# Performance work log

Measured on AMD Instinct MI355X. Metric: run time of the kernel, lower is better.

## Reference

```python
import jax, jax.numpy as jnp
import numpy as np

N = 100000          # num nodes
E = 1250000         # num directed edges
F_IN = 64           # num_features
H = 64              # hidden_channels
C = 2               # num_classes


def gcn_layer(x, W, b, src, dst, num_nodes):
    """PyG-style GCNConv: add self-loops, symmetric norm, scatter-add aggregation."""
    loop = jnp.arange(num_nodes)
    src2 = jnp.concatenate([src, loop])   # [E+N]
    dst2 = jnp.concatenate([dst, loop])
    deg = jax.ops.segment_sum(jnp.ones_like(dst2, dtype=x.dtype), dst2,
                              num_segments=num_nodes)          # in-degree incl self-loop
    dinv = jax.lax.rsqrt(jnp.maximum(deg, 1.0))                # deg >= 1 due to self-loops
    norm = dinv[src2] * dinv[dst2]                             # [E+N]
    h = x @ W                                                  # [N, out]
    out = jax.ops.segment_sum(norm[:, None] * h[src2], dst2,
                              num_segments=num_nodes)          # [N, out]
    return out + b


def setup_inputs() -> dict:
    key = jax.random.key(0)
    ks = jax.random.split(key, 8)
    x = jax.random.normal(ks[0], (N, F_IN), dtype=jnp.float32)
    edge_index = jax.random.randint(ks[1], (2, E), 0, N, dtype=jnp.int64)
    batch = jnp.zeros((N,), dtype=jnp.int64)
    s1 = 1.0 / np.sqrt(F_IN)
    s2 = 1.0 / np.sqrt(H)
    W1 = jax.random.uniform(ks[2], (F_IN, H), jnp.float32, -s1, s1)
    b1 = jnp.zeros((H,), jnp.float32)
    W2 = jax.random.uniform(ks[3], (H, H), jnp.float32, -s2, s2)
    b2 = jnp.zeros((H,), jnp.float32)
    Wlin = jax.random.uniform(ks[4], (H, C), jnp.float32, -s2, s2)
    blin = jax.random.uniform(ks[5], (C,), jnp.float32, -s2, s2)
    return {"x": x, "edge_index": edge_index, "batch": batch,
            "W1": W1, "b1": b1, "W2": W2, "b2": b2,
            "Wlin": Wlin, "blin": blin}


def reference(x, edge_index, batch, W1, b1, W2, b2, Wlin, blin):
    src, dst = edge_index[0], edge_index[1]
    h = gcn_layer(x, W1, b1, src, dst, N)
    h = jax.nn.relu(h)
    h = gcn_layer(h, W2, b2, src, dst, N)
    # dropout p=0.5 is identity in eval mode
    return h @ Wlin + blin  # [N, C]
```

## Files before the change

kernel.cpp:

```cpp
#include <hip/hip_runtime.h>
#include <hip/hip_bf16.h>


#define FDIM 64
#define BKT_BITS 9
#define BKT 512
#define CAP 8192
#define CHUNK 2048

typedef short s16x8 __attribute__((ext_vector_type(8)));
typedef float f32x4 __attribute__((ext_vector_type(4)));

__device__ __forceinline__ unsigned short f2b(float f) {
    unsigned u = __float_as_uint(f);
    u += 0x7fff + ((u >> 16) & 1);
    return (unsigned short)(u >> 16);
}
__device__ __forceinline__ void unpk(unsigned u, float& lo, float& hi) {
    lo = __uint_as_float(u << 16);
    hi = __uint_as_float(u & 0xffff0000u);
}
__device__ __forceinline__ unsigned packb(float lo, float hi) {
    return (unsigned)f2b(lo) | ((unsigned)f2b(hi) << 16);
}
__device__ __forceinline__ unsigned relu2(unsigned u) {
    unsigned t = (u >> 15) & 0x00010001u;
    return u & ~(t * 0xFFFFu);
}

__global__ __launch_bounds__(256) void k_zero_g(int* __restrict__ g, int nb) {
    int i = blockIdx.x * blockDim.x + threadIdx.x;
    if (i < nb) g[i] = 0;
}

__global__ __launch_bounds__(256) void k_part(const int* __restrict__ src,
                                              const int* __restrict__ dst,
                                              int* __restrict__ gcnt,
                                              unsigned* __restrict__ rec,
                                              int nE, int nb) {
    __shared__ int lh[256];
    __shared__ int rc[256];
    int t = threadIdx.x;
    if (t < nb) lh[t] = 0;
    __syncthreads();
    int e0 = blockIdx.x * CHUNK;
    int e1 = min(nE, e0 + CHUNK);
    int myb[8];
    unsigned myr[8];
#pragma unroll
    for (int j = 0; j < 8; ++j) {
        int i = e0 + t + j * 256;
        if (i < e1) {
            int d = dst[i];
            int s = src[i];
            int b = d >> BKT_BITS;
            myb[j] = b;
            myr[j] = (unsigned)s | ((unsigned)(d & (BKT - 1)) << 17);
            atomicAdd(&lh[b], 1);
        } else {
            myb[j] = -1;
        }
    }
    __syncthreads();
    if (t < nb) {
        int c = lh[t];
        rc[t] = t * CAP + (c ? atomicAdd(&gcnt[t], c) : 0);
    }
    __syncthreads();
#pragma unroll
    for (int j = 0; j < 8; ++j) {
        int b = myb[j];
        if (b >= 0) {
            int pos = atomicAdd(&rc[b], 1);
            if (pos < (b + 1) * CAP)
                rec[pos] = myr[j];
        }
    }
}

__global__ __launch_bounds__(256) void k_bscan(const int* __restrict__ gcnt,
                                               int* __restrict__ base,
                                               int* __restrict__ rowptr,
                                               int nb, int nE, int n) {
    int t = threadIdx.x;
    int b0 = t * 4;
    int v[4];
    int run = 0;
#pragma unroll
    for (int j = 0; j < 4; ++j) {
        int idx = b0 + j;
        int c = (idx < nb) ? gcnt[idx] : 0;
        v[j] = run;
        run += c;
    }
    int lane = t & 63, w = t >> 6;
    int inc = run;
#pragma unroll
    for (int off = 1; off < 64; off <<= 1) {
        int x = __shfl_up(inc, off);
        if (lane >= off) inc += x;
    }
    __shared__ int wt[4];
    if (lane == 63) wt[w] = inc;
    __syncthreads();
    int woff = 0;
    for (int i = 0; i < w; ++i) woff += wt[i];
    int gb = woff + (inc - run);
#pragma unroll
    for (int j = 0; j < 4; ++j) {
        int idx = b0 + j;
        if (idx < nb) base[idx] = gb + v[j];
    }
    if (t == 0) { base[nb] = nE; rowptr[n] = nE; }
}

__global__ __launch_bounds__(256) void k_bfill(const unsigned* __restrict__ rec,
                                               const int* __restrict__ gcnt,
                                               const int* __restrict__ base,
                                               int* __restrict__ rowptr,
                                               float* __restrict__ dinv,
                                               int* __restrict__ col, int n) {
    __shared__ int deg[BKT];
    __shared__ int cur[BKT];
    __shared__ int wt[4];
    int b = blockIdx.x, t = threadIdx.x;
    deg[t] = 0;
    deg[t + 256] = 0;
    __syncthreads();
    int rb = b * CAP;
    int re = rb + min(gcnt[b], CAP);
    for (int i = rb + t; i < re; i += 256)
        atomicAdd(&deg[rec[i] >> 17], 1);
    __syncthreads();
    {
        int d0 = deg[2 * t], d1 = deg[2 * t + 1];
        int run = d0 + d1;
        int lane = t & 63, w = t >> 6;
        int inc = run;
#pragma unroll
        for (int off = 1; off < 64; off <<= 1) {
            int x = __shfl_up(inc, off);
            if (lane >= off) inc += x;
        }
        if (lane == 63) wt[w] = inc;
        __syncthreads();
        int woff = 0;
        for (int i = 0; i < w; ++i) woff += wt[i];
        int ex = base[b] + woff + (inc - run);
        int off0 = ex, off1 = ex + d0;
        int node0 = b * BKT;
        int n0 = node0 + 2 * t, n1 = node0 + 2 * t + 1;
        if (n0 < n) { rowptr[n0] = off0; dinv[n0] = rsqrtf((float)(d0 + 1)); }
        if (n1 < n) { rowptr[n1] = off1; dinv[n1] = rsqrtf((float)(d1 + 1)); }
        cur[2 * t] = off0;
        cur[2 * t + 1] = off1;
    }
    __syncthreads();
    for (int i = rb + t; i < re; i += 256) {
        unsigned u = rec[i];
        int pos = atomicAdd(&cur[u >> 17], 1);
        col[pos] = (int)(u & 0x1FFFF);
    }
}

template <int INBF>
__global__ __launch_bounds__(256) void k_gemm_mfma(const void* __restrict__ Xv,
                                                   const float* __restrict__ W,
                                                   const float* __restrict__ dinv,
                                                   unsigned short* __restrict__ Yb,
                                                   int n) {
    int t = threadIdx.x, lane = t & 63;
    int ln = lane & 15;
    int kq = lane >> 4;
    int wave = (blockIdx.x * blockDim.x + t) >> 6;
    int nw = (gridDim.x * blockDim.x) >> 6;

    s16x8 bf[4][2];
#pragma unroll
    for (int nc = 0; nc < 4; ++nc) {
#pragma unroll
        for (int kc = 0; kc < 2; ++kc) {
            s16x8 s;
#pragma unroll
            for (int i = 0; i < 8; ++i) {
                int k = kc * 32 + kq * 8 + i;
                s[i] = (short)f2b(W[k * FDIM + nc * 16 + ln]);
            }
            bf[nc][kc] = s;
        }
    }

    int ntile = (n + 15) >> 4;
    for (int tile = wave; tile < ntile; tile += nw) {
        int rowbase = tile << 4;
        int arow = rowbase + ln;
        if (arow >= n) arow = n - 1;
        s16x8 a0, a1;
        if (INBF) {
            const unsigned short* Xb = (const unsigned short*)Xv;
            uint4 u0 = *(const uint4*)&Xb[(size_t)arow * FDIM + kq * 8];
            uint4 u1 = *(const uint4*)&Xb[(size_t)arow * FDIM + 32 + kq * 8];
            u0.x = relu2(u0.x); u0.y = relu2(u0.y); u0.z = relu2(u0.z); u0.w = relu2(u0.w);
            u1.x = relu2(u1.x); u1.y = relu2(u1.y); u1.z = relu2(u1.z); u1.w = relu2(u1.w);
            a0 = *reinterpret_cast<const s16x8*>(&u0);
            a1 = *reinterpret_cast<const s16x8*>(&u1);
        } else {
            const float* Xf = (const float*)Xv;
            const float* p = Xf + (size_t)arow * FDIM + kq * 8;
            float4 f0 = *(const float4*)p;
            float4 f1 = *(const float4*)(p + 4);
            float4 f2 = *(const float4*)(p + 32);
            float4 f3 = *(const float4*)(p + 36);
            a0[0] = (short)f2b(f0.x); a0[1] = (short)f2b(f0.y);
            a0[2] = (short)f2b(f0.z); a0[3] = (short)f2b(f0.w);
            a0[4] = (short)f2b(f1.x); a0[5] = (short)f2b(f1.y);
            a0[6] = (short)f2b(f1.z); a0[7] = (short)f2b(f1.w);
            a1[0] = (short)f2b(f2.x); a1[1] = (short)f2b(f2.y);
            a1[2] = (short)f2b(f2.z); a1[3] = (short)f2b(f2.w);
            a1[4] = (short)f2b(f3.x); a1[5] = (short)f2b(f3.y);
            a1[6] = (short)f2b(f3.z); a1[7] = (short)f2b(f3.w);
        }
        f32x4 acc[4];
#pragma unroll
        for (int nc = 0; nc < 4; ++nc) {
            f32x4 z = {0.f, 0.f, 0.f, 0.f};
            acc[nc] = __builtin_amdgcn_mfma_f32_16x16x32_bf16(a0, bf[nc][0], z, 0, 0, 0);
            acc[nc] = __builtin_amdgcn_mfma_f32_16x16x32_bf16(a1, bf[nc][1], acc[nc], 0, 0, 0);
        }
        int r0 = rowbase + kq * 4;
        float dd[4];
#pragma unroll
        for (int j = 0; j < 4; ++j) {
            int r = r0 + j;
            dd[j] = dinv[r < n ? r : (n - 1)];
        }
#pragma unroll
        for (int nc = 0; nc < 4; ++nc) {
#pragma unroll
            for (int j = 0; j < 4; ++j) {
                int r = r0 + j;
                if (r < n)
                    Yb[(size_t)r * FDIM + nc * 16 + ln] = f2b(acc[nc][j] * dd[j]);
            }
        }
    }
}

template <int HEAD>
__global__ __launch_bounds__(256) void k_gather(const unsigned short* __restrict__ Hsb,
                                                const float* __restrict__ dinv,
                                                const int* __restrict__ rowptr,
                                                const int* __restrict__ col,
                                                const float* __restrict__ bias,
                                                const float* __restrict__ Wlin,
                                                const float* __restrict__ blin,
                                                void* __restrict__ outp, int n) {
    int t = threadIdx.x, lane = t & 63;
    int g = lane >> 3;
    int fl = (lane & 7) * 8;
    int wave = (blockIdx.x * blockDim.x + t) >> 6;
    int nw = (gridDim.x * blockDim.x) >> 6;
    float4 blA = *(const float4*)&bias[fl];
    float4 blB = *(const float4*)&bias[fl + 4];
    float4 q0, q1, q2, q3;
    float bl0 = 0.f, bl1 = 0.f;
    if (HEAD) {
        q0 = *(const float4*)&Wlin[fl * 2];
        q1 = *(const float4*)&Wlin[fl * 2 + 4];
        q2 = *(const float4*)&Wlin[fl * 2 + 8];
        q3 = *(const float4*)&Wlin[fl * 2 + 12];
        bl0 = blin[0]; bl1 = blin[1];
    }
    for (int r0 = wave * 8; r0 < n; r0 += nw * 8) {
        int row = r0 + g;
        bool ok = row < n;
        int rr = ok ? row : (n - 1);
        int beg = rowptr[rr], end = rowptr[rr + 1];
        uint4 sv = *(const uint4*)&Hsb[(size_t)rr * FDIM + fl];
        float a0, a1, a2, a3, a4, a5, a6, a7;
        unpk(sv.x, a0, a1); unpk(sv.y, a2, a3);
        unpk(sv.z, a4, a5); unpk(sv.w, a6, a7);
        for (int k = beg; k < end; k += 8) {
            uint4 h[8];
#pragma unroll
            for (int j = 0; j < 8; ++j) {
                int kk = k + j;
                int s = col[kk < end ? kk : beg];
                h[j] = *(const uint4*)&Hsb[(size_t)s * FDIM + fl];
            }
#pragma unroll
            for (int j = 0; j < 8; ++j) {
                if (k + j < end) {
                    float l0, l1, l2, l3, l4, l5, l6, l7;
                    unpk(h[j].x, l0, l1); unpk(h[j].y, l2, l3);
                    unpk(h[j].z, l4, l5); unpk(h[j].w, l6, l7);
                    a0 += l0; a1 += l1; a2 += l2; a3 += l3;
                    a4 += l4; a5 += l5; a6 += l6; a7 += l7;
                }
            }
        }
        float dd = dinv[rr];
        float v0 = fmaf(dd, a0, blA.x), v1 = fmaf(dd, a1, blA.y);
        float v2 = fmaf(dd, a2, blA.z), v3 = fmaf(dd, a3, blA.w);
        float v4 = fmaf(dd, a4, blB.x), v5 = fmaf(dd, a5, blB.y);
        float v6 = fmaf(dd, a6, blB.z), v7 = fmaf(dd, a7, blB.w);
        if (HEAD == 0) {
            if (ok) {
                unsigned short* ob = (unsigned short*)outp;
                uint4 o;
                o.x = packb(v0, v1); o.y = packb(v2, v3);
                o.z = packb(v4, v5); o.w = packb(v6, v7);
                *(uint4*)&ob[(size_t)row * FDIM + fl] = o;
            }
        } else {
            float p0 = v0 * q0.x + v1 * q0.z + v2 * q1.x + v3 * q1.z
                     + v4 * q2.x + v5 * q2.z + v6 * q3.x + v7 * q3.z;
            float p1 = v0 * q0.y + v1 * q0.w + v2 * q1.y + v3 * q1.w
                     + v4 * q2.y + v5 * q2.w + v6 * q3.y + v7 * q3.w;
#pragma unroll
            for (int m = 4; m >= 1; m >>= 1) {
                p0 += __shfl_xor(p0, m);
                p1 += __shfl_xor(p1, m);
            }
            if (ok && (lane & 7) == 0) {
                float* of = (float*)outp;
                of[(size_t)row * 2 + 0] = p0 + bl0;
                of[(size_t)row * 2 + 1] = p1 + bl1;
            }
        }
    }
}

extern "C" void kernel_launch(void* const* d_in, const int* in_sizes, int n_in,
                              void* d_out, int out_size, void* d_ws, size_t ws_size,
                              hipStream_t stream) {
    const float* x    = (const float*)d_in[0];
    const int*   ei   = (const int*)d_in[1];
    const float* W1   = (const float*)d_in[3];
    const float* b1   = (const float*)d_in[4];
    const float* W2   = (const float*)d_in[5];
    const float* b2   = (const float*)d_in[6];
    const float* Wlin = (const float*)d_in[7];
    const float* blin = (const float*)d_in[8];
    float* out = (float*)d_out;

    const int n  = in_sizes[0] / FDIM;
    const int nE = in_sizes[1] / 2;
    const int* src = ei;
    const int* dst = ei + nE;
    const int NBUK = (n + BKT - 1) / BKT;

    int nPad = ((n + 1024) / 1024) * 1024;
    int nEPad = ((nE + 1023) / 1024) * 1024;
    int*      gcnt   = (int*)d_ws;
    int*      base   = gcnt + 1024;
    unsigned* rec    = (unsigned*)(base + 1024);
    int*      rowptr = (int*)(rec + (size_t)NBUK * CAP);
    float*    dinv   = (float*)(rowptr + nPad);
    int*      col    = (int*)(dinv + nPad);
    unsigned short* Hsb  = (unsigned short*)(col + nEPad);
    unsigned short* midb = Hsb + (size_t)nPad * FDIM;

    const int TB = 256;
    int blkP = (nE + CHUNK - 1) / CHUNK;

    k_zero_g<<<(NBUK + TB - 1) / TB, TB, 0, stream>>>(gcnt, NBUK);
    k_part<<<blkP, TB, 0, stream>>>(src, dst, gcnt, rec, nE, NBUK);
    k_bscan<<<1, TB, 0, stream>>>(gcnt, base, rowptr, NBUK, nE, n);
    k_bfill<<<NBUK, TB, 0, stream>>>(rec, gcnt, base, rowptr, dinv, col, n);

    k_gemm_mfma<0><<<512, TB, 0, stream>>>(x, W1, dinv, Hsb, n);
    k_gather<0><<<2048, TB, 0, stream>>>(Hsb, dinv, rowptr, col, b1, nullptr, nullptr, midb, n);

    k_gemm_mfma<1><<<512, TB, 0, stream>>>(midb, W2, dinv, Hsb, n);
    k_gather<1><<<2048, TB, 0, stream>>>(Hsb, dinv, rowptr, col, b2, Wlin, blin, out, n);

    (void)ws_size; (void)n_in; (void)out_size;
}
```

Before: 132.5 us.

## Fold bucket scan into fill kernel, halve buckets, prefetch gather column indices

Removes the single-block k_bscan launch. Each k_bfill block now computes its own base offset by summing the preceding bucket counts with one wave. Bucket size drops from 512 to 256 nodes, which doubles the number of fill blocks and gives one node per thread. The gather loop now software-pipelines the column-index loads, fetching the next 8 indices while the current rows are loaded, so the dependent-load latency is hidden. The cost is redundant prefix summation across blocks (up to ~390 reads per block) and more register pressure in the gather kernel.

```diff
diff --git a/kernel.cpp b/kernel.cpp
--- a/kernel.cpp
+++ b/kernel.cpp
@@ -3,9 +3,9 @@
 
 
 #define FDIM 64
-#define BKT_BITS 9
-#define BKT 512
-#define CAP 8192
+#define BKT_BITS 8
+#define BKT 256
+#define CAP 4096
 #define CHUNK 2048
 
 typedef short s16x8 __attribute__((ext_vector_type(8)));
@@ -38,10 +38,10 @@
                                               int* __restrict__ gcnt,
                                               unsigned* __restrict__ rec,
                                               int nE, int nb) {
-    __shared__ int lh[256];
-    __shared__ int rc[256];
+    __shared__ int lh[512];
+    __shared__ int rc[512];
     int t = threadIdx.x;
-    if (t < nb) lh[t] = 0;
+    for (int b = t; b < nb; b += 256) lh[b] = 0;
     __syncthreads();
     int e0 = blockIdx.x * CHUNK;
     int e1 = min(nE, e0 + CHUNK);
@@ -62,9 +62,9 @@
         }
     }
     __syncthreads();
-    if (t < nb) {
-        int c = lh[t];
-        rc[t] = t * CAP + (c ? atomicAdd(&gcnt[t], c) : 0);
+    for (int b = t; b < nb; b += 256) {
+        int c = lh[b];
+        rc[b] = b * CAP + (c ? atomicAdd(&gcnt[b], c) : 0);
     }
     __syncthreads();
 #pragma unroll
@@ -78,54 +78,26 @@
     }
 }
 
-__global__ __launch_bounds__(256) void k_bscan(const int* __restrict__ gcnt,
-                                               int* __restrict__ base,
-                                               int* __restrict__ rowptr,
-                                               int nb, int nE, int n) {
-    int t = threadIdx.x;
-    int b0 = t * 4;
-    int v[4];
-    int run = 0;
-#pragma unroll
-    for (int j = 0; j < 4; ++j) {
-        int idx = b0 + j;
-        int c = (idx < nb) ? gcnt[idx] : 0;
-        v[j] = run;
-        run += c;
-    }
-    int lane = t & 63, w = t >> 6;
-    int inc = run;
-#pragma unroll
-    for (int off = 1; off < 64; off <<= 1) {
-        int x = __shfl_up(inc, off);
-        if (lane >= off) inc += x;
-    }
-    __shared__ int wt[4];
-    if (lane == 63) wt[w] = inc;
-    __syncthreads();
-    int woff = 0;
-    for (int i = 0; i < w; ++i) woff += wt[i];
-    int gb = woff + (inc - run);
-#pragma unroll
-    for (int j = 0; j < 4; ++j) {
-        int idx = b0 + j;
-        if (idx < nb) base[idx] = gb + v[j];
-    }
-    if (t == 0) { base[nb] = nE; rowptr[n] = nE; }
-}
-
 __global__ __launch_bounds__(256) void k_bfill(const unsigned* __restrict__ rec,
                                                const int* __restrict__ gcnt,
-                                               const int* __restrict__ base,
                                                int* __restrict__ rowptr,
                                                float* __restrict__ dinv,
-                                               int* __restrict__ col, int n) {
+                                               int* __restrict__ col,
+                                               int n, int nb, int nE) {
     __shared__ int deg[BKT];
     __shared__ int cur[BKT];
     __shared__ int wt[4];
+    __shared__ int sbase;
     int b = blockIdx.x, t = threadIdx.x;
+    if (t < 64) {
+        int s = 0;
+        for (int i = t; i < b; i += 64) s += gcnt[i];
+#pragma unroll
+        for (int off = 32; off >= 1; off >>= 1) s += __shfl_xor(s, off);
+        if (t == 0) sbase = s;
+    }
     deg[t] = 0;
-    deg[t + 256] = 0;
+    if (b == nb - 1 && t == 0) rowptr[n] = nE;
     __syncthreads();
     int rb = b * CAP;
     int re = rb + min(gcnt[b], CAP);
@@ -133,10 +105,9 @@
         atomicAdd(&deg[rec[i] >> 17], 1);
     __syncthreads();
     {
-        int d0 = deg[2 * t], d1 = deg[2 * t + 1];
-        int run = d0 + d1;
+        int d0 = deg[t];
         int lane = t & 63, w = t >> 6;
-        int inc = run;
+        int inc = d0;
 #pragma unroll
         for (int off = 1; off < 64; off <<= 1) {
             int x = __shfl_up(inc, off);
@@ -146,14 +117,10 @@
         __syncthreads();
         int woff = 0;
         for (int i = 0; i < w; ++i) woff += wt[i];
-        int ex = base[b] + woff + (inc - run);
-        int off0 = ex, off1 = ex + d0;
-        int node0 = b * BKT;
-        int n0 = node0 + 2 * t, n1 = node0 + 2 * t + 1;
-        if (n0 < n) { rowptr[n0] = off0; dinv[n0] = rsqrtf((float)(d0 + 1)); }
-        if (n1 < n) { rowptr[n1] = off1; dinv[n1] = rsqrtf((float)(d1 + 1)); }
-        cur[2 * t] = off0;
-        cur[2 * t + 1] = off1;
+        int ex = sbase + woff + (inc - d0);
+        int node = b * BKT + t;
+        if (node < n) { rowptr[node] = ex; dinv[node] = rsqrtf((float)(d0 + 1)); }
+        cur[t] = ex;
     }
     __syncthreads();
     for (int i = rb + t; i < re; i += 256) {
@@ -280,14 +247,28 @@
         float a0, a1, a2, a3, a4, a5, a6, a7;
         unpk(sv.x, a0, a1); unpk(sv.y, a2, a3);
         unpk(sv.z, a4, a5); unpk(sv.w, a6, a7);
+        int c0[8];
+#pragma unroll
+        for (int j = 0; j < 8; ++j) c0[j] = 0;
+        if (beg < end) {
+#pragma unroll
+            for (int j = 0; j < 8; ++j) {
+                int kk = beg + j;
+                c0[j] = col[kk < end ? kk : beg];
+            }
+        }
         for (int k = beg; k < end; k += 8) {
+            int kn = k + 8;
+            int c1[8];
+#pragma unroll
+            for (int j = 0; j < 8; ++j) {
+                int kk = kn + j;
+                c1[j] = (kn < end) ? col[kk < end ? kk : kn] : 0;
+            }
             uint4 h[8];
 #pragma unroll
-            for (int j = 0; j < 8; ++j) {
-                int kk = k + j;
-                int s = col[kk < end ? kk : beg];
-                h[j] = *(const uint4*)&Hsb[(size_t)s * FDIM + fl];
-            }
+            for (int j = 0; j < 8; ++j)
+                h[j] = *(const uint4*)&Hsb[(size_t)c0[j] * FDIM + fl];
 #pragma unroll
             for (int j = 0; j < 8; ++j) {
                 if (k + j < end) {
@@ -298,6 +279,8 @@
                     a4 += l4; a5 += l5; a6 += l6; a7 += l7;
                 }
             }
+#pragma unroll
+            for (int j = 0; j < 8; ++j) c0[j] = c1[j];
         }
         float dd = dinv[rr];
         float v0 = fmaf(dd, a0, blA.x), v1 = fmaf(dd, a1, blA.y);
@@ -353,8 +336,7 @@
     int nPad = ((n + 1024) / 1024) * 1024;
     int nEPad = ((nE + 1023) / 1024) * 1024;
     int*      gcnt   = (int*)d_ws;
-    int*      base   = gcnt + 1024;
-    unsigned* rec    = (unsigned*)(base + 1024);
+    unsigned* rec    = (unsigned*)(gcnt + 1024);
     int*      rowptr = (int*)(rec + (size_t)NBUK * CAP);
     float*    dinv   = (float*)(rowptr + nPad);
     int*      col    = (int*)(dinv + nPad);
@@ -366,8 +348,7 @@
 
     k_zero_g<<<(NBUK + TB - 1) / TB, TB, 0, stream>>>(gcnt, NBUK);
     k_part<<<blkP, TB, 0, stream>>>(src, dst, gcnt, rec, nE, NBUK);
-    k_bscan<<<1, TB, 0, stream>>>(gcnt, base, rowptr, NBUK, nE, n);
-    k_bfill<<<NBUK, TB, 0, stream>>>(rec, gcnt, base, rowptr, dinv, col, n);
+    k_bfill<<<NBUK, TB, 0, stream>>>(rec, gcnt, rowptr, dinv, col, n, NBUK, nE);
 
     k_gemm_mfma<0><<<512, TB, 0, stream>>>(x, W1, dinv, Hsb, n);
     k_gather<0><<<2048, TB, 0, stream>>>(Hsb, dinv, rowptr, col, b1, nullptr, nullptr, midb, n);
```

Result: no change. 132.2 us (-0.2%).
